# Kernel optimization log

Measured on AMD Instinct MI355X. Metric: run time of the kernel, lower is better.

Reference implementation:

```python
import jax, jax.numpy as jnp
import numpy as np

N_NODES = 50000
N_EDGES = 800000
NEG_SLOPE = 0.2  # PyG GATv2Conv default
EPS = 1e-16      # PyG softmax denominator epsilon


def _segment_softmax(logits, seg, num_segments):
    # logits: [E, H]; seg: [E] target-node ids
    m = jax.ops.segment_max(logits, seg, num_segments=num_segments)
    p = jnp.exp(logits - m[seg])
    s = jax.ops.segment_sum(p, seg, num_segments=num_segments)
    return p / (s[seg] + EPS)


def _gatv2_conv(x, src, dst, Wl, Wr, att, bias, heads, out_ch, concat):
    # x: [N, F]; Wl/Wr: [F, heads*out_ch]; att: [heads, out_ch]
    n = x.shape[0]
    xl = (x @ Wl).reshape(n, heads, out_ch)
    xr = (x @ Wr).reshape(n, heads, out_ch)
    # GATv2: e_ij = att . leaky_relu(xl[j] + xr[i]) for edge j->i
    e = jax.nn.leaky_relu(xl[src] + xr[dst], NEG_SLOPE)  # [E, H, C]
    logit = jnp.einsum('ehc,hc->eh', e, att)             # [E, H]
    alpha = _segment_softmax(logit, dst, n)              # [E, H]
    out = jax.ops.segment_sum(alpha[:, :, None] * xl[src], dst, num_segments=n)  # [N, H, C]
    if concat:
        out = out.reshape(n, heads * out_ch)
    else:
        out = out.mean(axis=1)
    return out + bias


def setup_inputs() -> dict:
    key = jax.random.key(0)
    ks = jax.random.split(key, 20)
    in_ch, hid, out_ch, heads, edge_dim = 128, 128, 64, 8, 6
    c1 = hid // heads  # 16
    g = lambda k, shp, fan: (jax.random.normal(k, shp, jnp.float32) / np.sqrt(fan)).astype(jnp.float32)
    inp = {
        'x': jax.random.normal(ks[0], (N_NODES, in_ch), jnp.float32),
        'edge_index': jax.random.randint(ks[1], (2, N_EDGES), 0, N_NODES, dtype=jnp.int64),
        'edge_attr': jax.random.normal(ks[2], (N_EDGES, edge_dim), jnp.float32),
        'Wl1': g(ks[3], (in_ch, heads * c1), in_ch),
        'Wr1': g(ks[4], (in_ch, heads * c1), in_ch),
        'att1': g(ks[5], (heads, c1), c1),
        'b1': jnp.zeros((heads * c1,), jnp.float32),
        # layer 2: GATv2Conv(hid -> out_ch, heads=1, no concat)
        'Wl2': g(ks[6], (hid, out_ch), hid),
        'Wr2': g(ks[7], (hid, out_ch), hid),
        'att2': g(ks[8], (1, out_ch), out_ch),
        'b2': jnp.zeros((out_ch,), jnp.float32),
        # edge encoder (computed but unused downstream, as in the source)
        'We1': g(ks[9], (edge_dim, hid), edge_dim), 'be1': jnp.zeros((hid,), jnp.float32),
        'We2': g(ks[10], (hid, hid), hid), 'be2': jnp.zeros((hid,), jnp.float32),
        # classifier
        'Wc1': g(ks[11], (out_ch, hid), out_ch), 'bc1': jnp.zeros((hid,), jnp.float32),
        'Wc2': g(ks[12], (hid, 2), hid), 'bc2': jnp.zeros((2,), jnp.float32),
    }
    return inp


def reference(x, edge_index, edge_attr, Wl1, Wr1, att1, b1, Wl2, Wr2, att2, b2,
              We1, be1, We2, be2, Wc1, bc1, Wc2, bc2):
    n = x.shape[0]
    # edge encoder (dead code in the original forward; kept for fidelity)
    _edge_feats = jax.nn.relu(edge_attr @ We1 + be1) @ We2 + be2
    # add self-loops (PyG GATv2Conv default add_self_loops=True)
    loop = jnp.arange(n, dtype=edge_index.dtype)
    src = jnp.concatenate([edge_index[0], loop])
    dst = jnp.concatenate([edge_index[1], loop])
    # layer 1 (heads=8, concat) + relu; dropout is identity in eval
    h = _gatv2_conv(x, src, dst, Wl1, Wr1, att1, b1, heads=8, out_ch=16, concat=True)
    h = jax.nn.relu(h)
    # layer 2 (heads=1, mean)
    emb = _gatv2_conv(h, src, dst, Wl2, Wr2, att2, b2, heads=1, out_ch=64, concat=False)
    logits = jax.nn.relu(emb @ Wc1 + bc1) @ Wc2 + bc2
    return emb, logits
```

## Files before the change

### kernel.cpp

```cpp
#include <hip/hip_runtime.h>
#include <hip/hip_bf16.h>
#include <cfloat>

#define N_NODES 50000
#define N_EDGES 800000
#define E_TOT   850000
#define NEG_SLOPE 0.2f
#define SM_EPS 1e-16f
#define SCAN_B 196
#define LOG2E 1.4426950408889634f

typedef __attribute__((ext_vector_type(8))) short short8;
typedef __attribute__((ext_vector_type(4))) float f32x4;

__device__ __forceinline__ float lrelu(float v) { return v > 0.0f ? v : NEG_SLOPE * v; }

__device__ __forceinline__ unsigned f2bf_pack2(float a, float b) {
    unsigned ua = __float_as_uint(a);
    ua += 0x7fff + ((ua >> 16) & 1);
    unsigned ub = __float_as_uint(b);
    ub += 0x7fff + ((ub >> 16) & 1);
    return (ua >> 16) | (ub & 0xffff0000u);
}
__device__ __forceinline__ unsigned short f2bf(float a) {
    unsigned ua = __float_as_uint(a);
    ua += 0x7fff + ((ua >> 16) & 1);
    return (unsigned short)(ua >> 16);
}
__device__ __forceinline__ float bf_lo(unsigned u) { return __uint_as_float(u << 16); }
__device__ __forceinline__ float bf_hi(unsigned u) { return __uint_as_float(u & 0xffff0000u); }

__device__ __forceinline__ unsigned short pack_one(const float* __restrict__ B0,
                                                   const float* __restrict__ B1,
                                                   int i, int N) {
    int m   = i / (128 * N);
    int rem = i % (128 * N);
    int j    = rem & 7;
    int quad = (rem >> 3) & 3;
    int n    = (rem >> 5) & 15;
    int ctk  = rem >> 9;
    int ct   = ctk % (N / 16);
    int kt   = ctk / (N / 16);
    int k    = kt * 32 + quad * 8 + j;
    int col  = ct * 16 + n;
    const float* B = m ? B1 : B0;
    return f2bf(B[k * N + col]);
}

__global__ void prep(const float* __restrict__ Wl1, const float* __restrict__ Wr1,
                     const float* __restrict__ Wl2, const float* __restrict__ Wr2,
                     const float* __restrict__ Wc1,
                     unsigned short* __restrict__ Bp1, unsigned short* __restrict__ Bp2,
                     unsigned short* __restrict__ Wc1p,
                     int* __restrict__ deg, int* __restrict__ flags) {
    int i = blockIdx.x * 256 + threadIdx.x;
    if (i < 32768) {
        Bp1[i] = pack_one(Wl1, Wr1, i, 128);
    } else if (i < 49152) {
        Bp2[i - 32768] = pack_one(Wl2, Wr2, i - 32768, 64);
    } else if (i < 57344) {
        int idx = i - 49152;
        int j    = idx & 7;
        int quad = (idx >> 3) & 3;
        int n    = (idx >> 5) & 15;
        int ctk  = idx >> 9;
        int ct   = ctk & 7;
        int kt   = ctk >> 3;
        Wc1p[idx] = f2bf(Wc1[(kt * 32 + quad * 8 + j) * 128 + ct * 16 + n]);
    } else if (i < 107344) {
        deg[i - 57344] = 0;
    } else if (i < 107600) {
        flags[i - 107344] = 0;
    }
}

__device__ __forceinline__ void gemm128_half(int b, const float* __restrict__ x,
                                             const unsigned short* __restrict__ Bm,
                                             unsigned short* __restrict__ Cbf,
                                             float* __restrict__ Cf, int M) {
    int w = threadIdx.x >> 6, lane = threadIdx.x & 63;
    int quad = lane >> 4, l16 = lane & 15;
    int row0 = b * 32 + (w & 1) * 16;
    int cb   = (w >> 1) * 64;
    f32x4 acc[4];
    #pragma unroll
    for (int t = 0; t < 4; ++t) acc[t] = (f32x4){0.f, 0.f, 0.f, 0.f};
    int arow = row0 + l16;
    bool aok = arow < M;
    #pragma unroll
    for (int kt = 0; kt < 4; ++kt) {
        short8 a = (short8)0;
        if (aok) {
            const float* Ap = x + (size_t)arow * 128 + quad * 8 + kt * 32;
            float4 f0 = *(const float4*)(Ap);
            float4 f1 = *(const float4*)(Ap + 4);
            union { uint4 u; short8 s; } cv;
            cv.u.x = f2bf_pack2(f0.x, f0.y);
            cv.u.y = f2bf_pack2(f0.z, f0.w);
            cv.u.z = f2bf_pack2(f1.x, f1.y);
            cv.u.w = f2bf_pack2(f1.z, f1.w);
            a = cv.s;
        }
        #pragma unroll
        for (int t = 0; t < 4; ++t) {
            int ct = (cb >> 4) + t;
            const short* bp = (const short*)Bm + (((kt * 8 + ct) * 16 + l16) * 4 + quad) * 8;
            short8 bfr = *(const short8*)bp;
            acc[t] = __builtin_amdgcn_mfma_f32_16x16x32_bf16(a, bfr, acc[t], 0, 0, 0);
        }
    }
    #pragma unroll
    for (int t = 0; t < 4; ++t) {
        int col = cb + t * 16 + l16;
        #pragma unroll
        for (int r = 0; r < 4; ++r) {
            int row = row0 + quad * 4 + r;
            if (row < M) {
                if (Cbf) Cbf[(size_t)row * 128 + col] = f2bf(acc[t][r]);
                else     Cf[(size_t)row * 128 + col]  = acc[t][r];
            }
        }
    }
}

__global__ __launch_bounds__(256)
void k2_count_gemms(const int* __restrict__ ei, int* __restrict__ deg,
                    unsigned short* __restrict__ rank16,
                    const float* __restrict__ x, const unsigned short* __restrict__ Bp1,
                    unsigned short* __restrict__ xlbf, float* __restrict__ xr1, int M) {
    int kind = blockIdx.x % 3;
    int sub  = blockIdx.x / 3;
    if (kind == 1) {
        int nz = __syncthreads_or(ei[2 * threadIdx.x + 1]);
        int i = sub * 256 + threadIdx.x;
        if (2 * i >= N_EDGES) return;
        bool has2 = (2 * i + 1 < N_EDGES);
        int d0, d1 = 0;
        if (nz) {
            int2 dp = *(const int2*)(ei + N_EDGES + 2 * i);
            d0 = dp.x; d1 = dp.y;
        } else {
            int4 dp = *(const int4*)(ei + 2 * N_EDGES + 4 * i);
            d0 = dp.x; d1 = dp.z;
        }
        unsigned short r0 = (unsigned short)atomicAdd(&deg[d0], 1);
        unsigned short r1 = 0;
        if (has2) r1 = (unsigned short)atomicAdd(&deg[d1], 1);
        *(unsigned int*)(rank16 + 2 * i) = (unsigned int)r0 | ((unsigned int)r1 << 16);
    } else if (kind == 0) {
        gemm128_half(sub, x, Bp1, xlbf, nullptr, M);
    } else {
        gemm128_half(sub, x, Bp1 + 128 * 128, nullptr, xr1, M);
    }
}

__global__ void scan_fused(const int* __restrict__ deg, int* __restrict__ rowptr,
                           int* __restrict__ esrc, int* __restrict__ bsum,
                           int* __restrict__ flags) {
    __shared__ int sh[256];
    int b = blockIdx.x, t = threadIdx.x, i = b * 256 + t;
    int v = (i < N_NODES) ? deg[i] + 1 : 0;
    sh[t] = v;
    __syncthreads();
    int val = v;
    for (int off = 1; off < 256; off <<= 1) {
        int add = (t >= off) ? sh[t - off] : 0;
        __syncthreads();
        val += add; sh[t] = val;
        __syncthreads();
    }
    if (t == 255) {
        bsum[b] = val;
        __threadfence();
        atomicExch(&flags[b], 1);
    }
    int contrib = 0;
    if (t < b) {
        while (atomicAdd(&flags[t], 0) == 0) {}
        contrib = atomicAdd(&bsum[t], 0);
    }
    __syncthreads();
    sh[t] = contrib;
    __syncthreads();
    #pragma unroll
    for (int off = 128; off; off >>= 1) {
        if (t < off) sh[t] += sh[t + off];
        __syncthreads();
    }
    int offset = sh[0];
    if (i < N_NODES) {
        int rp = (val - v) + offset;
        rowptr[i] = rp;
        esrc[rp] = i;
    }
    if (i == 0) rowptr[N_NODES] = E_TOT;
}

__global__ void scatter_edges(const int* __restrict__ ei, const int* __restrict__ rowptr,
                              const unsigned short* __restrict__ rank16,
                              int* __restrict__ esrc) {
    int nz = __syncthreads_or(ei[2 * threadIdx.x + 1]);
    int i = blockIdx.x * blockDim.x + threadIdx.x;
    if (2 * i >= N_EDGES) return;
    bool has2 = (2 * i + 1 < N_EDGES);
    int s0, d0, s1 = 0, d1 = 0;
    if (nz) {
        int2 sp = *(const int2*)(ei + 2 * i);
        int2 dp = *(const int2*)(ei + N_EDGES + 2 * i);
        s0 = sp.x; s1 = sp.y; d0 = dp.x; d1 = dp.y;
    } else {
        int4 sp = *(const int4*)(ei + 4 * i);
        int4 dp = *(const int4*)(ei + 2 * N_EDGES + 4 * i);
        s0 = sp.x; s1 = sp.z; d0 = dp.x; d1 = dp.z;
    }
    unsigned int rr = *(const unsigned int*)(rank16 + 2 * i);
    esrc[rowptr[d0] + 1 + (int)(rr & 0xffffu)] = s0;
    if (has2) esrc[rowptr[d1] + 1 + (int)(rr >> 16)] = s1;
}

__global__ __launch_bounds__(256)
void gemm_mfma64(const unsigned short* __restrict__ Abf, const unsigned short* __restrict__ Bp,
                 unsigned short* __restrict__ C0bf, float* __restrict__ C1, int M) {
    int w = threadIdx.x >> 6, lane = threadIdx.x & 63;
    int quad = lane >> 4, l16 = lane & 15;
    int matrix = w >> 1;
    int row0 = blockIdx.x * 32 + (w & 1) * 16;
    const unsigned short* Bm = Bp + matrix * 128 * 64;
    f32x4 acc[4];
    #pragma unroll
    for (int t = 0; t < 4; ++t) acc[t] = (f32x4){0.f, 0.f, 0.f, 0.f};
    int arow = row0 + l16;
    bool aok = arow < M;
    const short* Ap = (const short*)Abf + (size_t)arow * 128 + quad * 8;
    #pragma unroll
    for (int kt = 0; kt < 4; ++kt) {
        short8 a = (short8)0;
        if (aok) a = *(const short8*)(Ap + kt * 32);
        #pragma unroll
        for (int t = 0; t < 4; ++t) {
            const short* bp = (const short*)Bm + (((kt * 4 + t) * 16 + l16) * 4 + quad) * 8;
            short8 bfr = *(const short8*)bp;
            acc[t] = __builtin_amdgcn_mfma_f32_16x16x32_bf16(a, bfr, acc[t], 0, 0, 0);
        }
    }
    #pragma unroll
    for (int t = 0; t < 4; ++t) {
        int col = t * 16 + l16;
        #pragma unroll
        for (int r = 0; r < 4; ++r) {
            int row = row0 + quad * 4 + r;
            if (row < M) {
                if (matrix) C1[(size_t)row * 64 + col] = acc[t][r];
                else        C0bf[(size_t)row * 64 + col] = f2bf(acc[t][r]);
            }
        }
    }
}

__global__ __launch_bounds__(256)
void node_fused1(const int* __restrict__ rowptr, const int* __restrict__ esrc,
                 const unsigned short* __restrict__ xlbf, const float* __restrict__ xr,
                 const float* __restrict__ att, const float* __restrict__ b1,
                 unsigned short* __restrict__ hbf) {
    int wave = threadIdx.x >> 6;
    int lane = threadIdx.x & 63;
    int n = blockIdx.x * 4 + wave;
    int slot = lane >> 4;
    int l = lane & 15;
    int beg = rowptr[n], end = rowptr[n + 1];
    const float* xrp = xr + (size_t)n * 128 + 8 * l;
    float4 xra = *(const float4*)(xrp);
    float4 xrb = *(const float4*)(xrp + 4);
    float4 ata = *(const float4*)(att + 8 * l);
    float4 atb = *(const float4*)(att + 8 * l + 4);
    ata.x *= LOG2E; ata.y *= LOG2E; ata.z *= LOG2E; ata.w *= LOG2E;
    atb.x *= LOG2E; atb.y *= LOG2E; atb.z *= LOG2E; atb.w *= LOG2E;
    float den = 0.0f;
    float4 aa = {0, 0, 0, 0}, ab = {0, 0, 0, 0};

    auto body = [&](int k) {
        int s = esrc[k];
        uint4 u = *(const uint4*)(xlbf + (size_t)s * 128 + 8 * l);
        float x0 = bf_lo(u.x), x1 = bf_hi(u.x);
        float x2 = bf_lo(u.y), x3 = bf_hi(u.y);
        float x4 = bf_lo(u.z), x5 = bf_hi(u.z);
        float x6 = bf_lo(u.w), x7 = bf_hi(u.w);
        float v = ata.x * lrelu(x0 + xra.x) + ata.y * lrelu(x1 + xra.y)
                + ata.z * lrelu(x2 + xra.z) + ata.w * lrelu(x3 + xra.w)
                + atb.x * lrelu(x4 + xrb.x) + atb.y * lrelu(x5 + xrb.y)
                + atb.z * lrelu(x6 + xrb.z) + atb.w * lrelu(x7 + xrb.w);
        v += __shfl_xor(v, 1);
        float p = exp2f(v);
        den += p;
        aa.x += p * x0; aa.y += p * x1; aa.z += p * x2; aa.w += p * x3;
        ab.x += p * x4; ab.y += p * x5; ab.z += p * x6; ab.w += p * x7;
    };
    int k = beg + slot;
    for (; k + 4 < end; k += 8) { body(k); body(k + 4); }
    if (k < end) body(k);

    #pragma unroll
    for (int off = 16; off < 64; off <<= 1) {
        aa.x += __shfl_xor(aa.x, off); aa.y += __shfl_xor(aa.y, off);
        aa.z += __shfl_xor(aa.z, off); aa.w += __shfl_xor(aa.w, off);
        ab.x += __shfl_xor(ab.x, off); ab.y += __shfl_xor(ab.y, off);
        ab.z += __shfl_xor(ab.z, off); ab.w += __shfl_xor(ab.w, off);
        den   += __shfl_xor(den, off);
    }
    if (slot == 0) {
        float inv = 1.0f / (den + SM_EPS);
        float4 b4a = *(const float4*)(b1 + 8 * l);
        float4 b4b = *(const float4*)(b1 + 8 * l + 4);
        float oa0 = fmaxf(aa.x * inv + b4a.x, 0.0f);
        float oa1 = fmaxf(aa.y * inv + b4a.y, 0.0f);
        float oa2 = fmaxf(aa.z * inv + b4a.z, 0.0f);
        float oa3 = fmaxf(aa.w * inv + b4a.w, 0.0f);
        float ob0 = fmaxf(ab.x * inv + b4b.x, 0.0f);
        float ob1 = fmaxf(ab.y * inv + b4b.y, 0.0f);
        float ob2 = fmaxf(ab.z * inv + b4b.z, 0.0f);
        float ob3 = fmaxf(ab.w * inv + b4b.w, 0.0f);
        uint4 pk;
        pk.x = f2bf_pack2(oa0, oa1);
        pk.y = f2bf_pack2(oa2, oa3);
        pk.z = f2bf_pack2(ob0, ob1);
        pk.w = f2bf_pack2(ob2, ob3);
        *(uint4*)(hbf + (size_t)n * 128 + 8 * l) = pk;
    }
}

__global__ __launch_bounds__(256)
void node_fused2(const int* __restrict__ rowptr, const int* __restrict__ esrc,
                 const unsigned short* __restrict__ xlbf, const float* __restrict__ xr,
                 const float* __restrict__ att, const float* __restrict__ b2v,
                 float* __restrict__ out_emb, unsigned short* __restrict__ embbf) {
    int wave = threadIdx.x >> 6;
    int lane = threadIdx.x & 63;
    int n = blockIdx.x * 4 + wave;
    int slot = lane >> 3;
    int l = lane & 7;
    int beg = rowptr[n], end = rowptr[n + 1];
    const float* xrp = xr + (size_t)n * 64 + 8 * l;
    float4 xra = *(const float4*)(xrp);
    float4 xrb = *(const float4*)(xrp + 4);
    float4 ata = *(const float4*)(att + 8 * l);
    float4 atb = *(const float4*)(att + 8 * l + 4);
    ata.x *= LOG2E; ata.y *= LOG2E; ata.z *= LOG2E; ata.w *= LOG2E;
    atb.x *= LOG2E; atb.y *= LOG2E; atb.z *= LOG2E; atb.w *= LOG2E;
    float den = 0.0f;
    float4 aa = {0, 0, 0, 0}, ab = {0, 0, 0, 0};

    auto body = [&](int k) {
        int s = esrc[k];
        uint4 u = *(const uint4*)(xlbf + (size_t)s * 64 + 8 * l);
        float x0 = bf_lo(u.x), x1 = bf_hi(u.x);
        float x2 = bf_lo(u.y), x3 = bf_hi(u.y);
        float x4 = bf_lo(u.z), x5 = bf_hi(u.z);
        float x6 = bf_lo(u.w), x7 = bf_hi(u.w);
        float v = ata.x * lrelu(x0 + xra.x) + ata.y * lrelu(x1 + xra.y)
                + ata.z * lrelu(x2 + xra.z) + ata.w * lrelu(x3 + xra.w)
                + atb.x * lrelu(x4 + xrb.x) + atb.y * lrelu(x5 + xrb.y)
                + atb.z * lrelu(x6 + xrb.z) + atb.w * lrelu(x7 + xrb.w);
        v += __shfl_xor(v, 1);
        v += __shfl_xor(v, 2);
        v += __shfl_xor(v, 4);
        float p = exp2f(v);
        den += p;
        aa.x += p * x0; aa.y += p * x1; aa.z += p * x2; aa.w += p * x3;
        ab.x += p * x4; ab.y += p * x5; ab.z += p * x6; ab.w += p * x7;
    };
    int k = beg + slot;
    for (; k + 8 < end; k += 16) { body(k); body(k + 8); }
    if (k < end) body(k);

    #pragma unroll
    for (int off = 8; off < 64; off <<= 1) {
        aa.x += __shfl_xor(aa.x, off); aa.y += __shfl_xor(aa.y, off);
        aa.z += __shfl_xor(aa.z, off); aa.w += __shfl_xor(aa.w, off);
        ab.x += __shfl_xor(ab.x, off); ab.y += __shfl_xor(ab.y, off);
        ab.z += __shfl_xor(ab.z, off); ab.w += __shfl_xor(ab.w, off);
        den   += __shfl_xor(den, off);
    }
    if (slot == 0) {
        float inv = 1.0f / (den + SM_EPS);
        float4 b4a = *(const float4*)(b2v + 8 * l);
        float4 b4b = *(const float4*)(b2v + 8 * l + 4);
        float4 ea, eb;
        ea.x = aa.x * inv + b4a.x; ea.y = aa.y * inv + b4a.y;
        ea.z = aa.z * inv + b4a.z; ea.w = aa.w * inv + b4a.w;
        eb.x = ab.x * inv + b4b.x; eb.y = ab.y * inv + b4b.y;
        eb.z = ab.z * inv + b4b.z; eb.w = ab.w * inv + b4b.w;
        float* op = out_emb + (size_t)n * 64 + 8 * l;
        *(float4*)(op)     = ea;
        *(float4*)(op + 4) = eb;
        uint4 pk;
        pk.x = f2bf_pack2(ea.x, ea.y);
        pk.y = f2bf_pack2(ea.z, ea.w);
        pk.z = f2bf_pack2(eb.x, eb.y);
        pk.w = f2bf_pack2(eb.z, eb.w);
        *(uint4*)(embbf + (size_t)n * 64 + 8 * l) = pk;
    }
}

__global__ __launch_bounds__(256)
void cls_mfma(const unsigned short* __restrict__ embbf, const unsigned short* __restrict__ Wc1p,
              const float* __restrict__ bc1, const float* __restrict__ Wc2,
              const float* __restrict__ bc2, float* __restrict__ out_logits) {
    __shared__ float part[2][16][2][2];
    int w = threadIdx.x >> 6, lane = threadIdx.x & 63;
    int quad = lane >> 4, l16 = lane & 15;
    int rowhalf = w & 1, colhalf = w >> 1;
    int row0 = blockIdx.x * 32 + rowhalf * 16;
    int cb = colhalf * 64;
    f32x4 acc[4];
    #pragma unroll
    for (int t = 0; t < 4; ++t) acc[t] = (f32x4){0.f, 0.f, 0.f, 0.f};
    int arow = row0 + l16;
    bool aok = arow < N_NODES;
    const short* Ap = (const short*)embbf + (size_t)arow * 64 + quad * 8;
    #pragma unroll
    for (int kt = 0; kt < 2; ++kt) {
        short8 a = (short8)0;
        if (aok) a = *(const short8*)(Ap + kt * 32);
        #pragma unroll
        for (int t = 0; t < 4; ++t) {
            int ct = colhalf * 4 + t;
            const short* bp = (const short*)Wc1p + (((kt * 8 + ct) * 16 + l16) * 4 + quad) * 8;
            short8 bfr = *(const short8*)bp;
            acc[t] = __builtin_amdgcn_mfma_f32_16x16x32_bf16(a, bfr, acc[t], 0, 0, 0);
        }
    }
    float p0[4] = {0, 0, 0, 0}, p1[4] = {0, 0, 0, 0};
    #pragma unroll
    for (int t = 0; t < 4; ++t) {
        int col = cb + t * 16 + l16;
        float w2a = Wc2[2 * col], w2b = Wc2[2 * col + 1];
        float bc = bc1[col];
        #pragma unroll
        for (int r = 0; r < 4; ++r) {
            float tv = fmaxf(acc[t][r] + bc, 0.0f);
            p0[r] += tv * w2a;
            p1[r] += tv * w2b;
        }
    }
    #pragma unroll
    for (int off = 1; off < 16; off <<= 1) {
        #pragma unroll
        for (int r = 0; r < 4; ++r) {
            p0[r] += __shfl_xor(p0[r], off);
            p1[r] += __shfl_xor(p1[r], off);
        }
    }
    if (l16 == 0) {
        #pragma unroll
        for (int r = 0; r < 4; ++r) {
            part[rowhalf][quad * 4 + r][colhalf][0] = p0[r];
            part[rowhalf][quad * 4 + r][colhalf][1] = p1[r];
        }
    }
    __syncthreads();
    int t = threadIdx.x;
    if (t < 64) {
        int row = t >> 1, c = t & 1;
        int rh = row >> 4, r16 = row & 15;
        float s = part[rh][r16][0][c] + part[rh][r16][1][c] + bc2[c];
        int n = blockIdx.x * 32 + row;
        if (n < N_NODES) out_logits[(size_t)n * 2 + c] = s;
    }
}

extern "C" void kernel_launch(void* const* d_in, const int* in_sizes, int n_in,
                              void* d_out, int out_size, void* d_ws, size_t ws_size,
                              hipStream_t stream) {
    const float* x    = (const float*)d_in[0];
    const int*   ei   = (const int*)d_in[1];
    const float* Wl1  = (const float*)d_in[3];
    const float* Wr1  = (const float*)d_in[4];
    const float* att1 = (const float*)d_in[5];
    const float* b1   = (const float*)d_in[6];
    const float* Wl2  = (const float*)d_in[7];
    const float* Wr2  = (const float*)d_in[8];
    const float* att2 = (const float*)d_in[9];
    const float* b2   = (const float*)d_in[10];
    const float* Wc1  = (const float*)d_in[15];
    const float* bc1  = (const float*)d_in[16];
    const float* Wc2  = (const float*)d_in[17];
    const float* bc2  = (const float*)d_in[18];

    float* ws = (float*)d_ws;
    int* deg    = (int*)ws;
    int* rowptr = deg + 50000;
    int* esrc   = rowptr + 50016;
    int* bsum   = esrc + 850000;
    int* flags  = bsum + 256;
    unsigned short* rank16 = (unsigned short*)(flags + 256);
    float* xr1           = ws + 1400448;
    unsigned short* xlbf = (unsigned short*)(ws + 7800448);
    unsigned short* hbf  = (unsigned short*)(ws + 11000448);
    unsigned short* Bp1   = (unsigned short*)(ws + 14200448);
    unsigned short* Bp2   = (unsigned short*)(ws + 14216832);
    unsigned short* Wc1p  = (unsigned short*)(ws + 14225024);
    unsigned short* embbf = (unsigned short*)(ws + 14229120);

    float* out_emb    = (float*)d_out;
    float* out_logits = out_emb + (size_t)N_NODES * 64;

    prep<<<421, 256, 0, stream>>>(Wl1, Wr1, Wl2, Wr2, Wc1, Bp1, Bp2, Wc1p, deg, flags);

    k2_count_gemms<<<4689, 256, 0, stream>>>(ei, deg, rank16, x, Bp1, xlbf, xr1, N_NODES);

    scan_fused<<<SCAN_B, 256, 0, stream>>>(deg, rowptr, esrc, bsum, flags);

    scatter_edges<<<1563, 256, 0, stream>>>(ei, rowptr, rank16, esrc);

    node_fused1<<<12500, 256, 0, stream>>>(rowptr, esrc, xlbf, xr1, att1, b1, hbf);

    gemm_mfma64<<<1563, 256, 0, stream>>>(hbf, Bp2, xlbf, xr1, N_NODES);
    node_fused2<<<12500, 256, 0, stream>>>(rowptr, esrc, xlbf, xr1, att2, b2, out_emb, embbf);

    cls_mfma<<<1563, 256, 0, stream>>>(embbf, Wc1p, bc1, Wc2, bc2, out_logits);
}
```

Measured before the change: 299.6 us.

## Privatize degree counters per XCD and fuse left/right GEMMs per block

Degree counting now uses eight per-XCD histogram copies with workgroup-scope relaxed atomics, tagging each rank with the XCD id so the scan can build per-XCD base offsets for scattering. This aims to cut cross-die atomic contention and coherence traffic. The layer-1 GEMM computes both Wl and Wr outputs in one block, so each x tile is loaded and converted once. Each count thread now handles four edges. Risks: workgroup-scope atomics on global memory are only correct if every block that shares an XCD copy sees coherent L2, the scan must read eight times more degree data, and a memset is added.

```diff
diff --git a/kernel.cpp b/kernel.cpp
--- a/kernel.cpp
+++ b/kernel.cpp
@@ -52,7 +52,7 @@
                      const float* __restrict__ Wc1,
                      unsigned short* __restrict__ Bp1, unsigned short* __restrict__ Bp2,
                      unsigned short* __restrict__ Wc1p,
-                     int* __restrict__ deg, int* __restrict__ flags) {
+                     int* __restrict__ flags) {
     int i = blockIdx.x * 256 + threadIdx.x;
     if (i < 32768) {
         Bp1[i] = pack_one(Wl1, Wr1, i, 128);
@@ -67,24 +67,25 @@
         int ct   = ctk & 7;
         int kt   = ctk >> 3;
         Wc1p[idx] = f2bf(Wc1[(kt * 32 + quad * 8 + j) * 128 + ct * 16 + n]);
-    } else if (i < 107344) {
-        deg[i - 57344] = 0;
-    } else if (i < 107600) {
-        flags[i - 107344] = 0;
-    }
-}
-
-__device__ __forceinline__ void gemm128_half(int b, const float* __restrict__ x,
-                                             const unsigned short* __restrict__ Bm,
-                                             unsigned short* __restrict__ Cbf,
-                                             float* __restrict__ Cf, int M) {
+    } else if (i < 57600) {
+        flags[i - 57344] = 0;
+    }
+}
+
+__device__ __forceinline__ void gemm128_both(int b, const float* __restrict__ x,
+                                             const unsigned short* __restrict__ Bp1,
+                                             unsigned short* __restrict__ xlbf,
+                                             float* __restrict__ xr1, int M) {
     int w = threadIdx.x >> 6, lane = threadIdx.x & 63;
     int quad = lane >> 4, l16 = lane & 15;
     int row0 = b * 32 + (w & 1) * 16;
     int cb   = (w >> 1) * 64;
-    f32x4 acc[4];
-    #pragma unroll
-    for (int t = 0; t < 4; ++t) acc[t] = (f32x4){0.f, 0.f, 0.f, 0.f};
+    f32x4 accL[4], accR[4];
+    #pragma unroll
+    for (int t = 0; t < 4; ++t) {
+        accL[t] = (f32x4){0.f, 0.f, 0.f, 0.f};
+        accR[t] = (f32x4){0.f, 0.f, 0.f, 0.f};
+    }
     int arow = row0 + l16;
     bool aok = arow < M;
     #pragma unroll
@@ -104,9 +105,11 @@
         #pragma unroll
         for (int t = 0; t < 4; ++t) {
             int ct = (cb >> 4) + t;
-            const short* bp = (const short*)Bm + (((kt * 8 + ct) * 16 + l16) * 4 + quad) * 8;
-            short8 bfr = *(const short8*)bp;
-            acc[t] = __builtin_amdgcn_mfma_f32_16x16x32_bf16(a, bfr, acc[t], 0, 0, 0);
+            const short* bp = (const short*)Bp1 + (((kt * 8 + ct) * 16 + l16) * 4 + quad) * 8;
+            short8 bL = *(const short8*)bp;
+            short8 bR = *(const short8*)(bp + 128 * 128);
+            accL[t] = __builtin_amdgcn_mfma_f32_16x16x32_bf16(a, bL, accL[t], 0, 0, 0);
+            accR[t] = __builtin_amdgcn_mfma_f32_16x16x32_bf16(a, bR, accR[t], 0, 0, 0);
         }
     }
     #pragma unroll
@@ -116,50 +119,65 @@
         for (int r = 0; r < 4; ++r) {
             int row = row0 + quad * 4 + r;
             if (row < M) {
-                if (Cbf) Cbf[(size_t)row * 128 + col] = f2bf(acc[t][r]);
-                else     Cf[(size_t)row * 128 + col]  = acc[t][r];
+                xlbf[(size_t)row * 128 + col] = f2bf(accL[t][r]);
+                xr1[(size_t)row * 128 + col]  = accR[t][r];
             }
         }
     }
 }
 
 __global__ __launch_bounds__(256)
-void k2_count_gemms(const int* __restrict__ ei, int* __restrict__ deg,
+void k2_count_gemms(const int* __restrict__ ei, unsigned* __restrict__ deg8,
                     unsigned short* __restrict__ rank16,
                     const float* __restrict__ x, const unsigned short* __restrict__ Bp1,
                     unsigned short* __restrict__ xlbf, float* __restrict__ xr1, int M) {
-    int kind = blockIdx.x % 3;
-    int sub  = blockIdx.x / 3;
-    if (kind == 1) {
+    int b = blockIdx.x;
+    int c = b / 3, rem = b % 3;
+    if (rem == 2) {
         int nz = __syncthreads_or(ei[2 * threadIdx.x + 1]);
-        int i = sub * 256 + threadIdx.x;
-        if (2 * i >= N_EDGES) return;
-        bool has2 = (2 * i + 1 < N_EDGES);
-        int d0, d1 = 0;
+        int i = c * 256 + threadIdx.x;
+        if (4 * i >= N_EDGES) return;
+        int d0, d1, d2, d3;
         if (nz) {
-            int2 dp = *(const int2*)(ei + N_EDGES + 2 * i);
-            d0 = dp.x; d1 = dp.y;
+            int4 dp = *(const int4*)(ei + N_EDGES + 4 * i);
+            d0 = dp.x; d1 = dp.y; d2 = dp.z; d3 = dp.w;
         } else {
-            int4 dp = *(const int4*)(ei + 2 * N_EDGES + 4 * i);
-            d0 = dp.x; d1 = dp.z;
-        }
-        unsigned short r0 = (unsigned short)atomicAdd(&deg[d0], 1);
-        unsigned short r1 = 0;
-        if (has2) r1 = (unsigned short)atomicAdd(&deg[d1], 1);
-        *(unsigned int*)(rank16 + 2 * i) = (unsigned int)r0 | ((unsigned int)r1 << 16);
-    } else if (kind == 0) {
-        gemm128_half(sub, x, Bp1, xlbf, nullptr, M);
+            int4 a0 = *(const int4*)(ei + 2 * N_EDGES + 8 * i);
+            int4 a1 = *(const int4*)(ei + 2 * N_EDGES + 8 * i + 4);
+            d0 = a0.x; d1 = a0.z; d2 = a1.x; d3 = a1.z;
+        }
+        unsigned xcd;
+        asm volatile("s_getreg_b32 %0, hwreg(HW_REG_XCC_ID)" : "=s"(xcd));
+        xcd &= 7u;
+        unsigned* dg = deg8 + xcd * 50000u;
+        unsigned tag = xcd << 13;
+        unsigned r0 = __hip_atomic_fetch_add(&dg[d0], 1u, __ATOMIC_RELAXED, __HIP_MEMORY_SCOPE_WORKGROUP);
+        unsigned r1 = __hip_atomic_fetch_add(&dg[d1], 1u, __ATOMIC_RELAXED, __HIP_MEMORY_SCOPE_WORKGROUP);
+        unsigned r2 = __hip_atomic_fetch_add(&dg[d2], 1u, __ATOMIC_RELAXED, __HIP_MEMORY_SCOPE_WORKGROUP);
+        unsigned r3 = __hip_atomic_fetch_add(&dg[d3], 1u, __ATOMIC_RELAXED, __HIP_MEMORY_SCOPE_WORKGROUP);
+        uint2 pk;
+        pk.x = (r0 | tag) | ((r1 | tag) << 16);
+        pk.y = (r2 | tag) | ((r3 | tag) << 16);
+        *(uint2*)(rank16 + 4 * i) = pk;
     } else {
-        gemm128_half(sub, x, Bp1 + 128 * 128, nullptr, xr1, M);
-    }
-}
-
-__global__ void scan_fused(const int* __restrict__ deg, int* __restrict__ rowptr,
+        int g = 2 * c + rem;
+        if (g >= 1563) return;
+        gemm128_both(g, x, Bp1, xlbf, xr1, M);
+    }
+}
+
+__global__ void scan_fused(const unsigned* __restrict__ deg8, int* __restrict__ rowptr,
                            int* __restrict__ esrc, int* __restrict__ bsum,
-                           int* __restrict__ flags) {
+                           int* __restrict__ flags, int* __restrict__ base8) {
     __shared__ int sh[256];
     int b = blockIdx.x, t = threadIdx.x, i = b * 256 + t;
-    int v = (i < N_NODES) ? deg[i] + 1 : 0;
+    unsigned d[8];
+    int tot = 0;
+    if (i < N_NODES) {
+        #pragma unroll
+        for (int xk = 0; xk < 8; ++xk) { d[xk] = deg8[xk * 50000 + i]; tot += (int)d[xk]; }
+    }
+    int v = (i < N_NODES) ? tot + 1 : 0;
     sh[t] = v;
     __syncthreads();
     int val = v;
@@ -192,11 +210,14 @@
         int rp = (val - v) + offset;
         rowptr[i] = rp;
         esrc[rp] = i;
+        int acc = rp + 1;
+        #pragma unroll
+        for (int xk = 0; xk < 8; ++xk) { base8[xk * 50000 + i] = acc; acc += (int)d[xk]; }
     }
     if (i == 0) rowptr[N_NODES] = E_TOT;
 }
 
-__global__ void scatter_edges(const int* __restrict__ ei, const int* __restrict__ rowptr,
+__global__ void scatter_edges(const int* __restrict__ ei, const int* __restrict__ base8,
                               const unsigned short* __restrict__ rank16,
                               int* __restrict__ esrc) {
     int nz = __syncthreads_or(ei[2 * threadIdx.x + 1]);
@@ -213,9 +234,10 @@
         int4 dp = *(const int4*)(ei + 2 * N_EDGES + 4 * i);
         s0 = sp.x; s1 = sp.z; d0 = dp.x; d1 = dp.z;
     }
-    unsigned int rr = *(const unsigned int*)(rank16 + 2 * i);
-    esrc[rowptr[d0] + 1 + (int)(rr & 0xffffu)] = s0;
-    if (has2) esrc[rowptr[d1] + 1 + (int)(rr >> 16)] = s1;
+    unsigned rr = *(const unsigned*)(rank16 + 2 * i);
+    unsigned r0 = rr & 0xffffu, r1 = rr >> 16;
+    esrc[base8[(r0 >> 13) * 50000 + d0] + (int)(r0 & 0x1fffu)] = s0;
+    if (has2) esrc[base8[(r1 >> 13) * 50000 + d1] + (int)(r1 & 0x1fffu)] = s1;
 }
 
 __global__ __launch_bounds__(256)
@@ -487,8 +509,7 @@
     const float* bc2  = (const float*)d_in[18];
 
     float* ws = (float*)d_ws;
-    int* deg    = (int*)ws;
-    int* rowptr = deg + 50000;
+    int* rowptr = (int*)ws + 50000;
     int* esrc   = rowptr + 50016;
     int* bsum   = esrc + 850000;
     int* flags  = bsum + 256;
@@ -496,6 +517,8 @@
     float* xr1           = ws + 1400448;
     unsigned short* xlbf = (unsigned short*)(ws + 7800448);
     unsigned short* hbf  = (unsigned short*)(ws + 11000448);
+    unsigned* deg8 = (unsigned*)(ws + 11000448);
+    int* base8     = (int*)(ws + 11400448);
     unsigned short* Bp1   = (unsigned short*)(ws + 14200448);
     unsigned short* Bp2   = (unsigned short*)(ws + 14216832);
     unsigned short* Wc1p  = (unsigned short*)(ws + 14225024);
@@ -504,13 +527,15 @@
     float* out_emb    = (float*)d_out;
     float* out_logits = out_emb + (size_t)N_NODES * 64;
 
-    prep<<<421, 256, 0, stream>>>(Wl1, Wr1, Wl2, Wr2, Wc1, Bp1, Bp2, Wc1p, deg, flags);
-
-    k2_count_gemms<<<4689, 256, 0, stream>>>(ei, deg, rank16, x, Bp1, xlbf, xr1, N_NODES);
-
-    scan_fused<<<SCAN_B, 256, 0, stream>>>(deg, rowptr, esrc, bsum, flags);
-
-    scatter_edges<<<1563, 256, 0, stream>>>(ei, rowptr, rank16, esrc);
+    hipMemsetAsync(deg8, 0, 400000 * sizeof(unsigned), stream);
+
+    prep<<<225, 256, 0, stream>>>(Wl1, Wr1, Wl2, Wr2, Wc1, Bp1, Bp2, Wc1p, flags);
+
+    k2_count_gemms<<<2346, 256, 0, stream>>>(ei, deg8, rank16, x, Bp1, xlbf, xr1, N_NODES);
+
+    scan_fused<<<SCAN_B, 256, 0, stream>>>(deg8, rowptr, esrc, bsum, flags, base8);
+
+    scatter_edges<<<1563, 256, 0, stream>>>(ei, base8, rank16, esrc);
 
     node_fused1<<<12500, 256, 0, stream>>>(rowptr, esrc, xlbf, xr1, att1, b1, hbf);
 
```

Result: no change. 296.2 us (-1.1%).
